# Performance work log

Measured on AMD Instinct MI355X. Metric: run time of the kernel, lower is better.

## Reference

```python
import jax, jax.numpy as jnp
import numpy as np

N_NODES = 100000
N_EDGES = 3200000  # avg degree 32
IN_DIM = 116       # fixed by GCNConv(116, hidden)
HIDDEN = 256


def setup_inputs() -> dict:
    key = jax.random.key(0)
    k1, k2, k3 = jax.random.split(key, 3)
    x = jax.random.normal(k1, (N_NODES, IN_DIM), dtype=jnp.float32)
    edge_index = jax.random.randint(k2, (2, N_EDGES), 0, N_NODES, dtype=jnp.int32)
    # GCNConv linear weight (stored here as [in, out]) and bias
    W = jax.random.normal(k3, (IN_DIM, HIDDEN), dtype=jnp.float32) * (1.0 / np.sqrt(IN_DIM))
    b = jnp.zeros((HIDDEN,), dtype=jnp.float32)
    return {"x": x, "edge_index": edge_index, "W": W, "b": b}


def reference(x, edge_index, W, b):
    # GCNConv: out = D^{-1/2} (A + I) D^{-1/2} (x W) + b ; then ReLU
    n = x.shape[0]
    loops = jnp.arange(n, dtype=edge_index.dtype)
    src = jnp.concatenate([edge_index[0], loops])  # [E + N]
    dst = jnp.concatenate([edge_index[1], loops])
    # degree of target nodes after self-loops (edge weight 1)
    deg = jax.ops.segment_sum(jnp.ones_like(src, dtype=x.dtype), dst, num_segments=n)
    dinv = jnp.where(deg > 0, jax.lax.rsqrt(deg), 0.0)
    norm = dinv[src] * dinv[dst]                   # [E + N]
    h = x @ W                                      # [N, H] project first (IN->H)
    msgs = h[src] * norm[:, None]                  # gather + scale
    agg = jax.ops.segment_sum(msgs, dst, num_segments=n)  # scatter-add
    return jax.nn.relu(agg + b)
```

## Files before the change

kernel.cpp:

```cpp
#include <hip/hip_runtime.h>


static constexpr int IN_DIM = 116;
static constexpr int PDIM   = 128;
static constexpr int HID    = 256;
static constexpr int BSH    = 8;
static constexpr int BNODES = 256;
static constexpr int NBPAD  = 512;
static constexpr int CHUNK  = 4096;
static constexpr int ECAP   = 9216;

typedef __attribute__((ext_vector_type(8))) short short8;
typedef __attribute__((ext_vector_type(4))) float f32x4;

__device__ __forceinline__ float bf_lo(uint u) { return __uint_as_float(u << 16); }
__device__ __forceinline__ float bf_hi(uint u) { return __uint_as_float(u & 0xffff0000u); }
__device__ __forceinline__ uint bf_pack(float a, float b) {
  uint ua = __float_as_uint(a); ua = (ua + 0x7fffu + ((ua >> 16) & 1u)) >> 16;
  uint ub = __float_as_uint(b); ub = (ub + 0x7fffu + ((ub >> 16) & 1u)) >> 16;
  return ua | (ub << 16);
}

__global__ __launch_bounds__(256) void k_bucket_hist(const int* __restrict__ dst, int E,
                                                     int* __restrict__ bcnt) {
  __shared__ int h[NBPAD];
  int tid = threadIdx.x;
  h[tid] = 0; h[tid + 256] = 0;
  __syncthreads();
  int stride = gridDim.x * 256;
  for (int e = blockIdx.x * 256 + tid; e < E; e += stride)
    atomicAdd(&h[dst[e] >> BSH], 1);
  __syncthreads();
  if (h[tid])       atomicAdd(&bcnt[tid], h[tid]);
  if (h[tid + 256]) atomicAdd(&bcnt[tid + 256], h[tid + 256]);
}

__global__ __launch_bounds__(256) void k_scan_b(const int* __restrict__ bcnt,
                                                int* __restrict__ bbase,
                                                int* __restrict__ bcursor) {
  __shared__ int s2[256];
  int t = threadIdx.x;
  int a = bcnt[2 * t], b = bcnt[2 * t + 1];
  s2[t] = a + b;
  __syncthreads();
  for (int off = 1; off < 256; off <<= 1) {
    int v = (t >= off) ? s2[t - off] : 0;
    __syncthreads();
    s2[t] += v;
    __syncthreads();
  }
  int ex2 = s2[t] - (a + b);
  bbase[2 * t] = ex2;         bcursor[2 * t] = ex2;
  bbase[2 * t + 1] = ex2 + a; bcursor[2 * t + 1] = ex2 + a;
}

__global__ __launch_bounds__(256) void k_scatter(const int* __restrict__ src,
                                                 const int* __restrict__ dst, int E,
                                                 int* __restrict__ bcursor,
                                                 int2* __restrict__ pairs) {
  __shared__ int hist[NBPAD];
  __shared__ int base[NBPAD];
  __shared__ int goff[NBPAD];
  __shared__ int s2[256];
  __shared__ int2 stage[CHUNK];
  int tid = threadIdx.x;
  int cbase = blockIdx.x * CHUNK;
  int cnt = E - cbase; if (cnt > CHUNK) cnt = CHUNK;
  hist[tid] = 0; hist[tid + 256] = 0;
  __syncthreads();

  int2 e[16]; int rk[16];
#pragma unroll
  for (int j = 0; j < 16; ++j) {
    int idx = cbase + j * 256 + tid;
    if (idx < E) {
      int d = dst[idx];
      e[j] = make_int2(d, src[idx]);
      rk[j] = atomicAdd(&hist[d >> BSH], 1);
    } else {
      e[j].x = -1;
    }
  }
  __syncthreads();
  {
    int a = hist[2 * tid], b = hist[2 * tid + 1];
    s2[tid] = a + b;
    __syncthreads();
    for (int off = 1; off < 256; off <<= 1) {
      int v = (tid >= off) ? s2[tid - off] : 0;
      __syncthreads();
      s2[tid] += v;
      __syncthreads();
    }
    int ex2 = s2[tid] - (a + b);
    base[2 * tid] = ex2; base[2 * tid + 1] = ex2 + a;
  }
  __syncthreads();
#pragma unroll
  for (int j = 0; j < 16; ++j)
    if (e[j].x >= 0) stage[base[e[j].x >> BSH] + rk[j]] = e[j];
  for (int b = tid; b < NBPAD; b += 256) {
    int c = hist[b];
    if (c > 0) goff[b] = atomicAdd(&bcursor[b], c);
  }
  __syncthreads();
  for (int i = tid; i < cnt; i += 256) {
    int2 v = stage[i];
    int b = v.x >> BSH;
    pairs[goff[b] + (i - base[b])] = v;
  }
}

__global__ __launch_bounds__(256) void k_deg(const int2* __restrict__ pairs,
                                             const int* __restrict__ bbase,
                                             const int* __restrict__ bcursor,
                                             int* __restrict__ deg,
                                             float* __restrict__ dinv, int n) {
  __shared__ int h[BNODES];
  int b = blockIdx.x, tid = threadIdx.x;
  h[tid] = 0;
  __syncthreads();
  int s = bbase[b], epos = bcursor[b];
  for (int e = s + tid; e < epos; e += 256)
    atomicAdd(&h[pairs[e].x & (BNODES - 1)], 1);
  __syncthreads();
  int v = (b << BSH) + tid;
  if (v < n) {
    int d = h[tid] + 1;
    deg[v] = d;
    dinv[v] = rsqrtf((float)d);
  }
}

__global__ __launch_bounds__(256) void k_scale(const float* __restrict__ x,
                                               const float* __restrict__ dinv,
                                               uint* __restrict__ xs, int n) {
  int gid = blockIdx.x * blockDim.x + threadIdx.x;
  int i = gid >> 4, q = gid & 15;
  if (i >= n) return;
  float dv = dinv[i];
  int c0 = q * 8;
  float c[8];
  if (c0 + 8 <= IN_DIM) {
    float4 v0 = *reinterpret_cast<const float4*>(x + (size_t)i * IN_DIM + c0);
    float4 v1 = *reinterpret_cast<const float4*>(x + (size_t)i * IN_DIM + c0 + 4);
    c[0] = v0.x; c[1] = v0.y; c[2] = v0.z; c[3] = v0.w;
    c[4] = v1.x; c[5] = v1.y; c[6] = v1.z; c[7] = v1.w;
  } else if (c0 < IN_DIM) {
    float4 v0 = *reinterpret_cast<const float4*>(x + (size_t)i * IN_DIM + c0);
    c[0] = v0.x; c[1] = v0.y; c[2] = v0.z; c[3] = v0.w;
    c[4] = c[5] = c[6] = c[7] = 0.f;
  } else {
    c[0] = c[1] = c[2] = c[3] = c[4] = c[5] = c[6] = c[7] = 0.f;
  }
#pragma unroll
  for (int j = 0; j < 8; ++j) c[j] *= dv;
  uint4 o;
  o.x = bf_pack(c[0], c[1]); o.y = bf_pack(c[2], c[3]);
  o.z = bf_pack(c[4], c[5]); o.w = bf_pack(c[6], c[7]);
  *reinterpret_cast<uint4*>(xs + (size_t)i * (PDIM / 2) + q * 4) = o;
}

__global__ __launch_bounds__(512) void k_agg2(const int2* __restrict__ pairs,
                                              const int* __restrict__ bbase,
                                              const int* __restrict__ bcursor,
                                              const int* __restrict__ deg,
                                              const float* __restrict__ dinv,
                                              const uint* __restrict__ xs,
                                              uint* __restrict__ aggb, int n) {
  __shared__ int srcs[ECAP];
  __shared__ int seg[BNODES + 1];
  __shared__ int cur[BNODES];
  __shared__ int sc[BNODES];
  int tid = threadIdx.x;
  int b = blockIdx.x;
  int node0 = b << BSH;
  int s = bbase[b], epos = bcursor[b];

  int len = 0;
  if (tid < BNODES) {
    int v = node0 + tid;
    len = (v < n) ? deg[v] - 1 : 0;
    sc[tid] = len;
  }
  __syncthreads();
  for (int off = 1; off < BNODES; off <<= 1) {
    int v = (tid < BNODES && tid >= off) ? sc[tid - off] : 0;
    __syncthreads();
    if (tid < BNODES) sc[tid] += v;
    __syncthreads();
  }
  if (tid < BNODES) { seg[tid] = sc[tid] - len; cur[tid] = sc[tid] - len; }
  if (tid == 0) seg[BNODES] = epos - s;
  __syncthreads();

  for (int e = s + tid; e < epos; e += 512) {
    int2 p = pairs[e];
    int pos = atomicAdd(&cur[p.x & (BNODES - 1)], 1);
    if (pos < ECAP) srcs[pos] = p.y;
  }
  __syncthreads();

  int wave = tid >> 6, lane = tid & 63;
  for (int i = 0; i < 32; ++i) {
    int vl = (wave << 5) + i;
    int v = node0 + vl;
    if (v >= n) continue;
    int s0 = seg[vl], s1 = seg[vl + 1];
    uint u = xs[(size_t)v * 64 + lane];
    float ax = bf_lo(u), ay = bf_hi(u);
    int e = s0;
    for (; e + 8 <= s1; e += 8) {
      int sj[8]; uint r[8];
#pragma unroll
      for (int j = 0; j < 8; ++j) sj[j] = srcs[e + j];
#pragma unroll
      for (int j = 0; j < 8; ++j) r[j] = xs[(size_t)sj[j] * 64 + lane];
#pragma unroll
      for (int j = 0; j < 8; ++j) { ax += bf_lo(r[j]); ay += bf_hi(r[j]); }
    }
    for (; e < s1; ++e) {
      uint r = xs[(size_t)srcs[e] * 64 + lane];
      ax += bf_lo(r); ay += bf_hi(r);
    }
    float dv = dinv[v];
    aggb[(size_t)v * 64 + lane] = bf_pack(ax * dv, ay * dv);
  }
}

__global__ __launch_bounds__(256) void k_prepw(const float* __restrict__ W,
                                               uint4* __restrict__ wfrag) {
  int t = blockIdx.x * 256 + threadIdx.x;
  int nc = t >> 8, ks = (t >> 6) & 3, l = t & 63;
  int kb = ks * 32 + (l >> 4) * 8;
  int c = nc * 16 + (l & 15);
  uint u[4];
#pragma unroll
  for (int p = 0; p < 4; ++p) {
    int k0 = kb + 2 * p, k1 = kb + 2 * p + 1;
    float f0 = (k0 < IN_DIM) ? W[(size_t)k0 * HID + c] : 0.f;
    float f1 = (k1 < IN_DIM) ? W[(size_t)k1 * HID + c] : 0.f;
    u[p] = bf_pack(f0, f1);
  }
  wfrag[t] = make_uint4(u[0], u[1], u[2], u[3]);
}

__global__ __launch_bounds__(256) void k_gemm_mfma(const uint4* __restrict__ aggb,
                                                   const uint4* __restrict__ wfrag,
                                                   const float* __restrict__ bias,
                                                   float* __restrict__ out, int n) {
  __shared__ uint4 At[128 * 16];
  int tid = threadIdx.x;
  int r0 = blockIdx.x * 128;

#pragma unroll
  for (int i = 0; i < 8; ++i) {
    int g = i * 256 + tid;
    int row = g >> 4, c = g & 15;
    int rr = r0 + row; if (rr >= n) rr = n - 1;
    At[row * 16 + (c ^ (row & 7))] = aggb[(size_t)rr * 16 + c];
  }
  __syncthreads();

  int wave = tid >> 6, lane = tid & 63;
  int lrow = lane & 15, lg = lane >> 4;
  int m0 = wave * 32;

  short8 a[2][4];
#pragma unroll
  for (int mf = 0; mf < 2; ++mf) {
    int row = m0 + mf * 16 + lrow;
#pragma unroll
    for (int ks = 0; ks < 4; ++ks) {
      int c = (ks * 4 + lg) ^ (row & 7);
      a[mf][ks] = *reinterpret_cast<const short8*>(&At[row * 16 + c]);
    }
  }

  f32x4 acc[2][16];
#pragma unroll
  for (int mf = 0; mf < 2; ++mf)
#pragma unroll
    for (int nc = 0; nc < 16; ++nc)
      acc[mf][nc] = (f32x4){0.f, 0.f, 0.f, 0.f};

#pragma unroll
  for (int nc = 0; nc < 16; ++nc) {
#pragma unroll
    for (int ks = 0; ks < 4; ++ks) {
      short8 bfr = *reinterpret_cast<const short8*>(&wfrag[(nc * 4 + ks) * 64 + lane]);
      acc[0][nc] = __builtin_amdgcn_mfma_f32_16x16x32_bf16(a[0][ks], bfr, acc[0][nc], 0, 0, 0);
      acc[1][nc] = __builtin_amdgcn_mfma_f32_16x16x32_bf16(a[1][ks], bfr, acc[1][nc], 0, 0, 0);
    }
  }

#pragma unroll
  for (int nc = 0; nc < 16; ++nc) {
    int col = nc * 16 + lrow;
    float bv = bias[col];
#pragma unroll
    for (int mf = 0; mf < 2; ++mf) {
#pragma unroll
      for (int r = 0; r < 4; ++r) {
        int rr = r0 + m0 + mf * 16 + lg * 4 + r;
        if (rr < n)
          out[(size_t)rr * HID + col] = fmaxf(acc[mf][nc][r] + bv, 0.f);
      }
    }
  }
}

extern "C" void kernel_launch(void* const* d_in, const int* in_sizes, int n_in,
                              void* d_out, int out_size, void* d_ws, size_t ws_size,
                              hipStream_t stream) {
  const float* x  = (const float*)d_in[0];
  const int*   ei = (const int*)d_in[1];
  const float* W  = (const float*)d_in[2];
  const float* bi = (const float*)d_in[3];
  float* out = (float*)d_out;

  int n = in_sizes[0] / IN_DIM;
  int E = in_sizes[1] / 2;
  const int* src = ei;
  const int* dst = ei + E;
  int NB = (n + BNODES - 1) >> BSH;

  char* p = (char*)d_ws;
  auto alloc = [&](size_t bytes) {
    char* r = p;
    p += (bytes + 255) & ~(size_t)255;
    return r;
  };
  int*   bcnt    = (int*)alloc(NBPAD * 4);
  int*   bbase   = (int*)alloc(NBPAD * 4);
  int*   bcursor = (int*)alloc(NBPAD * 4);
  int*   deg     = (int*)alloc((size_t)n * 4);
  float* dinv    = (float*)alloc((size_t)n * 4);
  int2*  pairs   = (int2*)alloc((size_t)E * 8);
  uint*  xs      = (uint*)alloc((size_t)n * (PDIM / 2) * 4);
  uint*  aggb    = (uint*)alloc((size_t)n * (PDIM / 2) * 4);
  uint4* wfrag   = (uint4*)alloc(4096 * 16);

  (void)hipMemsetAsync(bcnt, 0, NBPAD * 4, stream);

  int nchunks = (E + CHUNK - 1) / CHUNK;
  hipLaunchKernelGGL(k_bucket_hist, dim3(nchunks), dim3(256), 0, stream, dst, E, bcnt);
  hipLaunchKernelGGL(k_scan_b, dim3(1), dim3(256), 0, stream, bcnt, bbase, bcursor);
  hipLaunchKernelGGL(k_scatter, dim3(nchunks), dim3(256), 0, stream, src, dst, E, bcursor, pairs);
  hipLaunchKernelGGL(k_deg, dim3(NB), dim3(256), 0, stream, pairs, bbase, bcursor, deg, dinv, n);
  hipLaunchKernelGGL(k_scale, dim3((n * 16 + 255) / 256), dim3(256), 0, stream, x, dinv, xs, n);
  hipLaunchKernelGGL(k_prepw, dim3(16), dim3(256), 0, stream, W, wfrag);
  hipLaunchKernelGGL(k_agg2, dim3(NB), dim3(512), 0, stream,
                     pairs, bbase, bcursor, deg, dinv, xs, aggb, n);
  hipLaunchKernelGGL(k_gemm_mfma, dim3((n + 127) / 128), dim3(256), 0, stream,
                     (const uint4*)aggb, wfrag, bi, out, n);
}
```

Before: 422.7 us.

## Pack edge pairs into 32-bit words and build CSR for wave-per-node aggregation

Edge pairs are packed into one 32-bit word (8-bit local destination plus 24-bit source), which halves the scatter traffic. The degree kernel becomes a per-bucket counting sort that writes a global CSR array and row starts. Aggregation then runs one wave per node over that CSR, with no per-block shared-memory re-sort, and spreads across many more blocks with deeper unrolling. This adds an extra CSR write and read. It assumes node ids fit in 24 bits and still truncates bucket contents beyond ECAP.

```diff
diff --git a/kernel.cpp b/kernel.cpp
--- a/kernel.cpp
+++ b/kernel.cpp
@@ -57,28 +57,31 @@
 __global__ __launch_bounds__(256) void k_scatter(const int* __restrict__ src,
                                                  const int* __restrict__ dst, int E,
                                                  int* __restrict__ bcursor,
-                                                 int2* __restrict__ pairs) {
+                                                 uint* __restrict__ pairs) {
   __shared__ int hist[NBPAD];
   __shared__ int base[NBPAD];
   __shared__ int goff[NBPAD];
   __shared__ int s2[256];
-  __shared__ int2 stage[CHUNK];
+  __shared__ uint stage[CHUNK];
+  __shared__ unsigned short bkt[CHUNK];
   int tid = threadIdx.x;
   int cbase = blockIdx.x * CHUNK;
   int cnt = E - cbase; if (cnt > CHUNK) cnt = CHUNK;
   hist[tid] = 0; hist[tid + 256] = 0;
   __syncthreads();
 
-  int2 e[16]; int rk[16];
+  int db[16]; int rk[16]; uint pk[16];
 #pragma unroll
   for (int j = 0; j < 16; ++j) {
     int idx = cbase + j * 256 + tid;
     if (idx < E) {
       int d = dst[idx];
-      e[j] = make_int2(d, src[idx]);
-      rk[j] = atomicAdd(&hist[d >> BSH], 1);
+      int b = d >> BSH;
+      db[j] = b;
+      pk[j] = ((uint)(d & (BNODES - 1)) << 24) | (uint)src[idx];
+      rk[j] = atomicAdd(&hist[b], 1);
     } else {
-      e[j].x = -1;
+      db[j] = -1;
     }
   }
   __syncthreads();
@@ -98,38 +101,64 @@
   __syncthreads();
 #pragma unroll
   for (int j = 0; j < 16; ++j)
-    if (e[j].x >= 0) stage[base[e[j].x >> BSH] + rk[j]] = e[j];
+    if (db[j] >= 0) {
+      int pos = base[db[j]] + rk[j];
+      stage[pos] = pk[j];
+      bkt[pos] = (unsigned short)db[j];
+    }
   for (int b = tid; b < NBPAD; b += 256) {
     int c = hist[b];
     if (c > 0) goff[b] = atomicAdd(&bcursor[b], c);
   }
   __syncthreads();
   for (int i = tid; i < cnt; i += 256) {
-    int2 v = stage[i];
-    int b = v.x >> BSH;
-    pairs[goff[b] + (i - base[b])] = v;
-  }
-}
-
-__global__ __launch_bounds__(256) void k_deg(const int2* __restrict__ pairs,
-                                             const int* __restrict__ bbase,
-                                             const int* __restrict__ bcursor,
-                                             int* __restrict__ deg,
-                                             float* __restrict__ dinv, int n) {
+    int b = bkt[i];
+    pairs[goff[b] + (i - base[b])] = stage[i];
+  }
+}
+
+__global__ __launch_bounds__(256) void k_sort(const uint* __restrict__ pairs,
+                                              const int* __restrict__ bbase,
+                                              const int* __restrict__ bcursor,
+                                              int* __restrict__ row_start,
+                                              float* __restrict__ dinv,
+                                              int* __restrict__ csr, int n) {
   __shared__ int h[BNODES];
+  __shared__ int sc[BNODES];
+  __shared__ int cur[BNODES];
+  __shared__ int stage[ECAP];
   int b = blockIdx.x, tid = threadIdx.x;
   h[tid] = 0;
   __syncthreads();
   int s = bbase[b], epos = bcursor[b];
   for (int e = s + tid; e < epos; e += 256)
-    atomicAdd(&h[pairs[e].x & (BNODES - 1)], 1);
-  __syncthreads();
+    atomicAdd(&h[pairs[e] >> 24], 1);
+  __syncthreads();
+  int len = h[tid];
+  sc[tid] = len;
+  __syncthreads();
+  for (int off = 1; off < 256; off <<= 1) {
+    int t = (tid >= off) ? sc[tid - off] : 0;
+    __syncthreads();
+    sc[tid] += t;
+    __syncthreads();
+  }
+  int ex = sc[tid] - len;
+  cur[tid] = ex;
   int v = (b << BSH) + tid;
   if (v < n) {
-    int d = h[tid] + 1;
-    deg[v] = d;
-    dinv[v] = rsqrtf((float)d);
-  }
+    row_start[v] = s + ex;
+    dinv[v] = rsqrtf((float)(len + 1));
+  }
+  __syncthreads();
+  for (int e = s + tid; e < epos; e += 256) {
+    uint p = pairs[e];
+    int pos = atomicAdd(&cur[p >> 24], 1);
+    if (pos < ECAP) stage[pos] = (int)(p & 0xFFFFFFu);
+  }
+  __syncthreads();
+  int cnt = epos - s; if (cnt > ECAP) cnt = ECAP;
+  for (int i = tid; i < cnt; i += 256) csr[s + i] = stage[i];
 }
 
 __global__ __launch_bounds__(256) void k_scale(const float* __restrict__ x,
@@ -161,71 +190,44 @@
   *reinterpret_cast<uint4*>(xs + (size_t)i * (PDIM / 2) + q * 4) = o;
 }
 
-__global__ __launch_bounds__(512) void k_agg2(const int2* __restrict__ pairs,
-                                              const int* __restrict__ bbase,
-                                              const int* __restrict__ bcursor,
-                                              const int* __restrict__ deg,
+__global__ __launch_bounds__(256) void k_agg3(const int* __restrict__ csr,
+                                              const int* __restrict__ row_start,
                                               const float* __restrict__ dinv,
                                               const uint* __restrict__ xs,
-                                              uint* __restrict__ aggb, int n) {
-  __shared__ int srcs[ECAP];
-  __shared__ int seg[BNODES + 1];
-  __shared__ int cur[BNODES];
-  __shared__ int sc[BNODES];
-  int tid = threadIdx.x;
-  int b = blockIdx.x;
-  int node0 = b << BSH;
-  int s = bbase[b], epos = bcursor[b];
-
-  int len = 0;
-  if (tid < BNODES) {
-    int v = node0 + tid;
-    len = (v < n) ? deg[v] - 1 : 0;
-    sc[tid] = len;
-  }
-  __syncthreads();
-  for (int off = 1; off < BNODES; off <<= 1) {
-    int v = (tid < BNODES && tid >= off) ? sc[tid - off] : 0;
-    __syncthreads();
-    if (tid < BNODES) sc[tid] += v;
-    __syncthreads();
-  }
-  if (tid < BNODES) { seg[tid] = sc[tid] - len; cur[tid] = sc[tid] - len; }
-  if (tid == 0) seg[BNODES] = epos - s;
-  __syncthreads();
-
-  for (int e = s + tid; e < epos; e += 512) {
-    int2 p = pairs[e];
-    int pos = atomicAdd(&cur[p.x & (BNODES - 1)], 1);
-    if (pos < ECAP) srcs[pos] = p.y;
-  }
-  __syncthreads();
-
-  int wave = tid >> 6, lane = tid & 63;
-  for (int i = 0; i < 32; ++i) {
-    int vl = (wave << 5) + i;
-    int v = node0 + vl;
-    if (v >= n) continue;
-    int s0 = seg[vl], s1 = seg[vl + 1];
-    uint u = xs[(size_t)v * 64 + lane];
-    float ax = bf_lo(u), ay = bf_hi(u);
-    int e = s0;
-    for (; e + 8 <= s1; e += 8) {
-      int sj[8]; uint r[8];
-#pragma unroll
-      for (int j = 0; j < 8; ++j) sj[j] = srcs[e + j];
-#pragma unroll
-      for (int j = 0; j < 8; ++j) r[j] = xs[(size_t)sj[j] * 64 + lane];
-#pragma unroll
-      for (int j = 0; j < 8; ++j) { ax += bf_lo(r[j]); ay += bf_hi(r[j]); }
-    }
-    for (; e < s1; ++e) {
-      uint r = xs[(size_t)srcs[e] * 64 + lane];
-      ax += bf_lo(r); ay += bf_hi(r);
-    }
-    float dv = dinv[v];
-    aggb[(size_t)v * 64 + lane] = bf_pack(ax * dv, ay * dv);
-  }
+                                              uint* __restrict__ aggb, int n, int E) {
+  int gw = (blockIdx.x * 256 + threadIdx.x) >> 6;
+  int lane = threadIdx.x & 63;
+  if (gw >= n) return;
+  int v = gw;
+  int s0 = row_start[v];
+  int s1 = (v + 1 < n) ? row_start[v + 1] : E;
+  uint u = xs[(size_t)v * 64 + lane];
+  float ax = bf_lo(u), ay = bf_hi(u);
+  int e = s0;
+  for (; e + 16 <= s1; e += 16) {
+    int sj[16]; uint r[16];
+#pragma unroll
+    for (int j = 0; j < 16; ++j) sj[j] = csr[e + j];
+#pragma unroll
+    for (int j = 0; j < 16; ++j) r[j] = xs[(size_t)sj[j] * 64 + lane];
+#pragma unroll
+    for (int j = 0; j < 16; ++j) { ax += bf_lo(r[j]); ay += bf_hi(r[j]); }
+  }
+  for (; e + 4 <= s1; e += 4) {
+    int sj[4]; uint r[4];
+#pragma unroll
+    for (int j = 0; j < 4; ++j) sj[j] = csr[e + j];
+#pragma unroll
+    for (int j = 0; j < 4; ++j) r[j] = xs[(size_t)sj[j] * 64 + lane];
+#pragma unroll
+    for (int j = 0; j < 4; ++j) { ax += bf_lo(r[j]); ay += bf_hi(r[j]); }
+  }
+  for (; e < s1; ++e) {
+    uint r = xs[(size_t)csr[e] * 64 + lane];
+    ax += bf_lo(r); ay += bf_hi(r);
+  }
+  float dv = dinv[v];
+  aggb[(size_t)v * 64 + lane] = bf_pack(ax * dv, ay * dv);
 }
 
 __global__ __launch_bounds__(256) void k_prepw(const float* __restrict__ W,
@@ -331,15 +333,16 @@
     p += (bytes + 255) & ~(size_t)255;
     return r;
   };
-  int*   bcnt    = (int*)alloc(NBPAD * 4);
-  int*   bbase   = (int*)alloc(NBPAD * 4);
-  int*   bcursor = (int*)alloc(NBPAD * 4);
-  int*   deg     = (int*)alloc((size_t)n * 4);
-  float* dinv    = (float*)alloc((size_t)n * 4);
-  int2*  pairs   = (int2*)alloc((size_t)E * 8);
-  uint*  xs      = (uint*)alloc((size_t)n * (PDIM / 2) * 4);
-  uint*  aggb    = (uint*)alloc((size_t)n * (PDIM / 2) * 4);
-  uint4* wfrag   = (uint4*)alloc(4096 * 16);
+  int*   bcnt      = (int*)alloc(NBPAD * 4);
+  int*   bbase     = (int*)alloc(NBPAD * 4);
+  int*   bcursor   = (int*)alloc(NBPAD * 4);
+  int*   row_start = (int*)alloc((size_t)n * 4);
+  float* dinv      = (float*)alloc((size_t)n * 4);
+  uint*  pairs     = (uint*)alloc((size_t)E * 4);
+  int*   csr       = (int*)alloc((size_t)E * 4);
+  uint*  xs        = (uint*)alloc((size_t)n * (PDIM / 2) * 4);
+  uint*  aggb      = (uint*)alloc((size_t)n * (PDIM / 2) * 4);
+  uint4* wfrag     = (uint4*)alloc(4096 * 16);
 
   (void)hipMemsetAsync(bcnt, 0, NBPAD * 4, stream);
 
@@ -347,11 +350,12 @@
   hipLaunchKernelGGL(k_bucket_hist, dim3(nchunks), dim3(256), 0, stream, dst, E, bcnt);
   hipLaunchKernelGGL(k_scan_b, dim3(1), dim3(256), 0, stream, bcnt, bbase, bcursor);
   hipLaunchKernelGGL(k_scatter, dim3(nchunks), dim3(256), 0, stream, src, dst, E, bcursor, pairs);
-  hipLaunchKernelGGL(k_deg, dim3(NB), dim3(256), 0, stream, pairs, bbase, bcursor, deg, dinv, n);
+  hipLaunchKernelGGL(k_sort, dim3(NB), dim3(256), 0, stream,
+                     pairs, bbase, bcursor, row_start, dinv, csr, n);
   hipLaunchKernelGGL(k_scale, dim3((n * 16 + 255) / 256), dim3(256), 0, stream, x, dinv, xs, n);
   hipLaunchKernelGGL(k_prepw, dim3(16), dim3(256), 0, stream, W, wfrag);
-  hipLaunchKernelGGL(k_agg2, dim3(NB), dim3(512), 0, stream,
-                     pairs, bbase, bcursor, deg, dinv, xs, aggb, n);
+  hipLaunchKernelGGL(k_agg3, dim3((n * 64 + 255) / 256), dim3(256), 0, stream,
+                     csr, row_start, dinv, xs, aggb, n, E);
   hipLaunchKernelGGL(k_gemm_mfma, dim3((n + 127) / 128), dim3(256), 0, stream,
                      (const uint4*)aggb, wfrag, bi, out, n);
 }
```

New measurement: 390.1 us. 7.7% less time.
